# Performance work log

Hardware: AMD Instinct MI355X
Metric: run time of the kernel (lower is better)

The kernel has to match this reference:

```python
import jax, jax.numpy as jnp
import numpy as np

N_HEADS = 16
ROPE_BASE = 10000.0
EPS = float(np.finfo(np.float32).eps)  # F.rms_norm default eps for fp32


def _rms_norm(x):
    # RMSNorm over last dim, no learned scale (modded-nanogpt `norm`)
    return x * jax.lax.rsqrt(jnp.mean(jnp.square(x), axis=-1, keepdims=True) + EPS)


def _rotary(x):
    # x: [B, T, H, D]; non-interleaved half-rotation as in the Rotary module
    B, T, H, D = x.shape
    inv_freq = (1.0 / ROPE_BASE) ** (jnp.arange(0, D, 2, dtype=jnp.float32) / D)  # [D/2]
    t = jnp.arange(T, dtype=jnp.float32)
    freqs = jnp.outer(t, inv_freq)  # [T, D/2]
    cos = jnp.cos(freqs)[None, :, None, :]
    sin = jnp.sin(freqs)[None, :, None, :]
    x1, x2 = jnp.split(x, 2, axis=3)
    y1 = x1 * cos + x2 * sin
    y2 = -x1 * sin + x2 * cos
    return jnp.concatenate((y1, y2), axis=3).astype(x.dtype)


def setup_inputs() -> dict:
    key = jax.random.key(0)
    k1, k2, k3, k4 = jax.random.split(key, 4)
    B, T, Hs = 1, 2048, 2048
    d_head = Hs // N_HEADS
    std = 0.5 * d_head ** (-0.5)
    bound = 3 ** 0.5 * std
    x = jax.random.normal(k1, (B, T, Hs), dtype=jnp.float32)
    Wqkv = jax.random.uniform(k2, (3, Hs, Hs), dtype=jnp.float32, minval=-bound, maxval=bound)
    Wo_w = jax.random.normal(k3, (Hs, Hs), dtype=jnp.float32) * (Hs ** -0.5)
    Wo_b = jax.random.normal(k4, (Hs,), dtype=jnp.float32) * 0.01
    return {"x": x, "Wqkv": Wqkv, "Wo_w": Wo_w, "Wo_b": Wo_b}


def reference(x, Wqkv, Wo_w, Wo_b):
    B, T, Hs = x.shape
    d_head = Hs // N_HEADS
    # fused QKV projection: F.linear(x, Wqkv.flatten(end_dim=1)) -> x @ W^T
    W = Wqkv.reshape(3 * Hs, Hs)
    qkv = jnp.einsum('bth,oh->bto', x, W).reshape(B, T, 3 * N_HEADS, d_head)
    q, k, v = jnp.split(qkv, 3, axis=-2)  # each [B, T, H, D]
    q, k = _rms_norm(q), _rms_norm(k)
    q, k = _rotary(q), _rotary(k)
    # causal attention (flex_attention block_mask = causal), scale = 1/sqrt(d)
    scale = 1.0 / jnp.sqrt(jnp.float32(d_head))
    scores = jnp.einsum('bthd,bshd->bhts', q, k) * scale  # [B, H, T, S]
    causal = jnp.tril(jnp.ones((T, T), dtype=bool))
    scores = jnp.where(causal[None, None], scores, jnp.float32(-1e30))
    probs = jax.nn.softmax(scores, axis=-1)
    y = jnp.einsum('bhts,bshd->bthd', probs, v).reshape(B, T, Hs)
    return jnp.einsum('bth,oh->bto', y, Wo_w) + Wo_b
```

## Files before the change

### kernel.cpp

```cpp
#include <hip/hip_runtime.h>
#include <hip/hip_bf16.h>
#include <stdint.h>

#define T_SEQ 2048
#define HS    2048
#define NH    16
#define DH    128
#define QKVN  (3*HS)

typedef __attribute__((ext_vector_type(8))) short          bf16x8;
typedef __attribute__((ext_vector_type(4))) float          f32x4;
typedef __attribute__((ext_vector_type(4))) unsigned short us4;
typedef __attribute__((ext_vector_type(8))) unsigned short us8;

__device__ __forceinline__ unsigned short f2bf(float x) {
  unsigned int u = __float_as_uint(x);
  return (unsigned short)((u + 0x7fffu + ((u >> 16) & 1u)) >> 16);
}

__device__ __forceinline__ void gl_lds16(const void* g, void* l) {
  __builtin_amdgcn_global_load_lds((__attribute__((address_space(1))) void*)g,
                                   (__attribute__((address_space(3))) void*)l, 16, 0, 0);
}

__global__ __launch_bounds__(256) void cast_bf16_kernel(const float* __restrict__ in,
                                                        unsigned short* __restrict__ out, int n) {
  int i = (blockIdx.x * 256 + threadIdx.x) * 8;
  if (i >= n) return;
  f32x4 a = *(const f32x4*)(in + i);
  f32x4 b = *(const f32x4*)(in + i + 4);
  us8 r;
#pragma unroll
  for (int j = 0; j < 4; ++j) { r[j] = f2bf(a[j]); r[j + 4] = f2bf(b[j]); }
  *(us8*)(out + i) = r;
}

__global__ __launch_bounds__(256) void rope_table_kernel(float* __restrict__ cosd,
                                                         float* __restrict__ sind) {
  int i = blockIdx.x * 256 + threadIdx.x;
  if (i >= T_SEQ * 64) return;
  int t = i >> 6, f = i & 63;
  float inv = expf(-9.210340371976184f * (float)f * (1.0f / 64.0f));
  float ang = (float)t * inv;
  float s, c;
  sincosf(ang, &s, &c);
  cosd[i] = c; sind[i] = s;
}

template <int BIAS, int BN>
__global__ __launch_bounds__(256, 4)
void gemm_bt(const unsigned short* __restrict__ A, const unsigned short* __restrict__ Bt,
             float* __restrict__ C, const float* __restrict__ bias, int M, int N, int K) {
  constexpr int FN = BN / 32;
  __shared__ unsigned short As[128 * 64];
  __shared__ unsigned short Bs[BN * 64];
  const int tid  = threadIdx.x;
  const int lane = tid & 63;
  const int w    = tid >> 6;
  const int fr   = lane & 15;
  const int fq   = lane >> 4;
  const int bm   = blockIdx.y * 128;
  const int bn   = blockIdx.x * BN;
  const int wr   = (w >> 1) * 64;
  const int wc   = (w & 1) * (BN / 2);

  f32x4 acc[4][FN];
#pragma unroll
  for (int m = 0; m < 4; ++m)
#pragma unroll
    for (int n = 0; n < FN; ++n) { acc[m][n][0]=0.f; acc[m][n][1]=0.f; acc[m][n][2]=0.f; acc[m][n][3]=0.f; }

  const int srow = lane >> 3;
  const int sg   = (lane & 7) ^ srow;
  const unsigned short* Ag = A + (long)bm * K;
  const unsigned short* Bg = Bt + (long)bn * K;

  const int nk = K >> 6;
  for (int kt = 0; kt < nk; ++kt) {
    const int k0 = kt << 6;
    __syncthreads();
#pragma unroll
    for (int i = 0; i < 4; ++i) {
      int r = i * 32 + w * 8;
      gl_lds16(Ag + (long)(r + srow) * K + k0 + sg * 8, &As[r * 64]);
    }
#pragma unroll
    for (int i = 0; i < BN / 32; ++i) {
      int r = i * 32 + w * 8;
      gl_lds16(Bg + (long)(r + srow) * K + k0 + sg * 8, &Bs[r * 64]);
    }
    __syncthreads();
    __builtin_amdgcn_s_setprio(1);
#pragma unroll
    for (int ks = 0; ks < 2; ++ks) {
      bf16x8 af[4], bfr[FN];
#pragma unroll
      for (int m = 0; m < 4; ++m)
        af[m]  = *(const bf16x8*)&As[(wr + m * 16 + fr) * 64 + (((ks * 4 + fq) ^ (fr & 7)) << 3)];
#pragma unroll
      for (int n = 0; n < FN; ++n)
        bfr[n] = *(const bf16x8*)&Bs[(wc + n * 16 + fr) * 64 + (((ks * 4 + fq) ^ (fr & 7)) << 3)];
#pragma unroll
      for (int m = 0; m < 4; ++m)
#pragma unroll
        for (int n = 0; n < FN; ++n)
          acc[m][n] = __builtin_amdgcn_mfma_f32_16x16x32_bf16(af[m], bfr[n], acc[m][n], 0, 0, 0);
    }
    __builtin_amdgcn_s_setprio(0);
  }
#pragma unroll
  for (int m = 0; m < 4; ++m) {
    int row0 = bm + wr + m * 16 + fq * 4;
#pragma unroll
    for (int n = 0; n < FN; ++n) {
      int col = bn + wc + n * 16 + fr;
      float bv = BIAS ? bias[col] : 0.0f;
#pragma unroll
      for (int j = 0; j < 4; ++j)
        C[(long)(row0 + j) * N + col] = acc[m][n][j] + bv;
    }
  }
}

__global__ __launch_bounds__(256)
void normrope_qk(const float* __restrict__ qkv, const float* __restrict__ cosd,
                 const float* __restrict__ sind, unsigned short* __restrict__ qb,
                 unsigned short* __restrict__ kb) {
  const int wgl  = (blockIdx.x * 256 + threadIdx.x) >> 6;
  const int lane = threadIdx.x & 63;
  for (int rr = wgl; rr < T_SEQ * 32; rr += 4096) {
    const int t = rr >> 5;
    const int y = rr & 31;
    const float2 v = *(const float2*)(qkv + (long)t * QKVN + y * 128 + lane * 2);
    float ss = v.x * v.x + v.y * v.y;
#pragma unroll
    for (int m = 1; m < 64; m <<= 1) ss += __shfl_xor(ss, m, 64);
    const float r = rsqrtf(ss * (1.0f / 128.0f) + 1.1920928955078125e-07f);
    const float a = v.x * r, b = v.y * r;
    const float pa = __shfl_xor(a, 32, 64), pb = __shfl_xor(b, 32, 64);
    const float2 c2 = *(const float2*)(cosd + t * 64 + (lane & 31) * 2);
    const float2 s2 = *(const float2*)(sind + t * 64 + (lane & 31) * 2);
    float o0, o1;
    if (lane < 32) { o0 =  a * c2.x + pa * s2.x;  o1 =  b * c2.y + pb * s2.y; }
    else           { o0 = -pa * s2.x + a * c2.x;  o1 = -pb * s2.y + b * c2.y; }
    unsigned short* dst = (y >> 4) ? kb : qb;
    const unsigned int packed = (unsigned int)f2bf(o0) | ((unsigned int)f2bf(o1) << 16);
    *(unsigned int*)(dst + ((long)(y & 15) * T_SEQ + t) * 128 + lane * 2) = packed;
  }
}

__global__ __launch_bounds__(256)
void v_transpose(const float* __restrict__ qkv, unsigned short* __restrict__ vt) {
  const int tb = blockIdx.x;
  const int h  = blockIdx.y;
  __shared__ unsigned short vl[128][72];
  const int tid = threadIdx.x;
#pragma unroll
  for (int p = 0; p < 32; ++p) {
    int rr = p * 2 + (tid >> 7);
    int d  = tid & 127;
    float x = qkv[(long)(tb * 64 + rr) * QKVN + 2 * HS + h * 128 + d];
    vl[d][rr] = f2bf(x);
  }
  __syncthreads();
#pragma unroll
  for (int p = 0; p < 8; ++p) {
    int idx = (p * 256 + tid) * 4;
    int d = idx >> 6;
    int i = idx & 63;
    us4 val = *(const us4*)&vl[d][i];
    *(us4*)&vt[((long)h * DH + d) * T_SEQ + tb * 64 + i] = val;
  }
}

__global__ __launch_bounds__(256, 2)
void attn_kernel(const unsigned short* __restrict__ qg, const unsigned short* __restrict__ kg,
                 const unsigned short* __restrict__ vtg, unsigned short* __restrict__ yb) {
  const int bi = blockIdx.x;
  const int j  = (bi < 256) ? bi : bi - 256;
  const int h  = j & 15;
  const int q0 = j >> 4;
  const int qb = (bi < 256) ? (31 - q0) : q0;

  __shared__ unsigned short Ks[2][64 * 128];
  __shared__ unsigned short Vts[2][128 * 64];
  __shared__ unsigned short Ps[4][16 * 72];

  const int tid = threadIdx.x, lane = tid & 63, w = tid >> 6;
  const int fr = lane & 15, fq = lane >> 4;

  const unsigned short* qh = qg  + (long)h * T_SEQ * 128;
  const unsigned short* kh = kg  + (long)h * T_SEQ * 128;
  const unsigned short* vh = vtg + (long)h * 128 * T_SEQ;

  const int krow_off = lane >> 4;
  const int vrow_off = lane >> 3;
  const int vg       = (lane & 7) ^ vrow_off;

  {
#pragma unroll
    for (int i = 0; i < 4; ++i) {
      int c = w * 4 + i;
      int r = 4 * c + krow_off;
      int g = (lane & 15) ^ (r & 7);
      gl_lds16(kh + r * 128 + g * 8, &Ks[0][c * 512]);
    }
#pragma unroll
    for (int i = 0; i < 4; ++i) {
      int r0 = (w * 4 + i) * 8;
      gl_lds16(vh + (long)(r0 + vrow_off) * T_SEQ + vg * 8, &Vts[0][r0 * 64]);
    }
  }

  bf16x8 aq[4];
  {
    const unsigned short* qrow = qh + (long)(qb * 64 + w * 16 + fr) * 128;
#pragma unroll
    for (int ks = 0; ks < 4; ++ks)
      aq[ks] = *(const bf16x8*)(qrow + ks * 32 + fq * 8);
  }

  f32x4 acc[8];
#pragma unroll
  for (int n = 0; n < 8; ++n) { acc[n][0]=0.f; acc[n][1]=0.f; acc[n][2]=0.f; acc[n][3]=0.f; }
  float mrow[4], lrow[4];
#pragma unroll
  for (int j2 = 0; j2 < 4; ++j2) { mrow[j2] = -__builtin_huge_valf(); lrow[j2] = 0.f; }

  const float scale = 0.08838834764831845f;

  __syncthreads();

  for (int kt = 0; kt <= qb; ++kt) {
    const int cur = kt & 1;

    if (kt < qb) {
      const int nb = cur ^ 1;
      const unsigned short* ksrc = kh + (kt + 1) * (64 * 128);
      const unsigned short* vsrc = vh + (kt + 1) * 64;
#pragma unroll
      for (int i = 0; i < 4; ++i) {
        int c = w * 4 + i;
        int r = 4 * c + krow_off;
        int g = (lane & 15) ^ (r & 7);
        gl_lds16(ksrc + r * 128 + g * 8, &Ks[nb][c * 512]);
      }
#pragma unroll
      for (int i = 0; i < 4; ++i) {
        int r0 = (w * 4 + i) * 8;
        gl_lds16(vsrc + (long)(r0 + vrow_off) * T_SEQ + vg * 8, &Vts[nb][r0 * 64]);
      }
    }

    f32x4 sv[4];
#pragma unroll
    for (int n = 0; n < 4; ++n) { sv[n][0]=0.f; sv[n][1]=0.f; sv[n][2]=0.f; sv[n][3]=0.f; }
    __builtin_amdgcn_s_setprio(1);
#pragma unroll
    for (int ks = 0; ks < 4; ++ks)
#pragma unroll
      for (int n = 0; n < 4; ++n) {
        int R = n * 16 + fr;
        bf16x8 bk = *(const bf16x8*)&Ks[cur][R * 128 + (((ks * 4 + fq) ^ (fr & 7)) << 3)];
        sv[n] = __builtin_amdgcn_mfma_f32_16x16x32_bf16(aq[ks], bk, sv[n], 0, 0, 0);
      }
    __builtin_amdgcn_s_setprio(0);

#pragma unroll
    for (int n = 0; n < 4; ++n)
#pragma unroll
      for (int j3 = 0; j3 < 4; ++j3) {
        float s = sv[n][j3] * scale;
        if (kt == qb && (n * 16 + fr) > (w * 16 + fq * 4 + j3)) s = -__builtin_huge_valf();
        sv[n][j3] = s;
      }

    float pm[4];
#pragma unroll
    for (int j3 = 0; j3 < 4; ++j3)
      pm[j3] = fmaxf(fmaxf(sv[0][j3], sv[1][j3]), fmaxf(sv[2][j3], sv[3][j3]));
#pragma unroll
    for (int m = 1; m < 16; m <<= 1)
#pragma unroll
      for (int j3 = 0; j3 < 4; ++j3) pm[j3] = fmaxf(pm[j3], __shfl_xor(pm[j3], m, 64));

    float alpha[4];
#pragma unroll
    for (int j3 = 0; j3 < 4; ++j3) {
      float mn = fmaxf(mrow[j3], pm[j3]);
      alpha[j3] = __expf(mrow[j3] - mn);
      mrow[j3] = mn;
    }
    float rs[4] = {0.f, 0.f, 0.f, 0.f};
#pragma unroll
    for (int n = 0; n < 4; ++n)
#pragma unroll
      for (int j3 = 0; j3 < 4; ++j3) {
        float p = __expf(sv[n][j3] - mrow[j3]);
        sv[n][j3] = p;
        rs[j3] += p;
      }
#pragma unroll
    for (int m = 1; m < 16; m <<= 1)
#pragma unroll
      for (int j3 = 0; j3 < 4; ++j3) rs[j3] += __shfl_xor(rs[j3], m, 64);
#pragma unroll
    for (int j3 = 0; j3 < 4; ++j3) lrow[j3] = lrow[j3] * alpha[j3] + rs[j3];
#pragma unroll
    for (int n = 0; n < 8; ++n)
#pragma unroll
      for (int j3 = 0; j3 < 4; ++j3) acc[n][j3] *= alpha[j3];

    unsigned short* pl = &Ps[w][0];
#pragma unroll
    for (int n = 0; n < 4; ++n)
#pragma unroll
      for (int j3 = 0; j3 < 4; ++j3)
        pl[(fq * 4 + j3) * 72 + n * 16 + fr] = f2bf(sv[n][j3]);
    asm volatile("s_waitcnt lgkmcnt(0)" ::: "memory");
    __builtin_amdgcn_s_setprio(1);
#pragma unroll
    for (int ks = 0; ks < 2; ++ks) {
      bf16x8 pa = *(const bf16x8*)&pl[fr * 72 + ks * 32 + fq * 8];
#pragma unroll
      for (int n = 0; n < 8; ++n) {
        int R = n * 16 + fr;
        bf16x8 bv = *(const bf16x8*)&Vts[cur][R * 64 + (((ks * 4 + fq) ^ (fr & 7)) << 3)];
        acc[n] = __builtin_amdgcn_mfma_f32_16x16x32_bf16(pa, bv, acc[n], 0, 0, 0);
      }
    }
    __builtin_amdgcn_s_setprio(0);

    __syncthreads();
  }

#pragma unroll
  for (int j3 = 0; j3 < 4; ++j3) {
    float inv = 1.0f / lrow[j3];
    int t = qb * 64 + w * 16 + fq * 4 + j3;
#pragma unroll
    for (int n = 0; n < 8; ++n)
      yb[(long)t * HS + h * 128 + n * 16 + fr] = f2bf(acc[n][j3] * inv);
  }
}

extern "C" void kernel_launch(void* const* d_in, const int* in_sizes, int n_in,
                              void* d_out, int out_size, void* d_ws, size_t ws_size,
                              hipStream_t stream) {
  const float* x    = (const float*)d_in[0];
  const float* Wqkv = (const float*)d_in[1];
  const float* Wo_w = (const float*)d_in[2];
  const float* Wo_b = (const float*)d_in[3];
  float* out = (float*)d_out;
  char* ws = (char*)d_ws;

  unsigned short* xbf  = (unsigned short*)(ws + 0L);
  unsigned short* wqbf = (unsigned short*)(ws + 8388608L);
  unsigned short* wobf = (unsigned short*)(ws + 33554432L);
  float*          qkv  = (float*)         (ws + 41943040L);
  unsigned short* qb   = (unsigned short*)(ws + 92274688L);
  unsigned short* kb   = (unsigned short*)(ws + 100663296L);
  unsigned short* vt   = (unsigned short*)(ws + 109051904L);
  unsigned short* yb   = (unsigned short*)(ws + 117440512L);
  float*          cosd = (float*)         (ws + 125829120L);
  float*          sind = (float*)         (ws + 126353408L);

  cast_bf16_kernel<<<dim3(4194304 / 8 / 256), 256, 0, stream>>>(x, xbf, 4194304);
  cast_bf16_kernel<<<dim3(12582912 / 8 / 256), 256, 0, stream>>>(Wqkv, wqbf, 12582912);
  cast_bf16_kernel<<<dim3(4194304 / 8 / 256), 256, 0, stream>>>(Wo_w, wobf, 4194304);
  rope_table_kernel<<<dim3(512), 256, 0, stream>>>(cosd, sind);

  gemm_bt<0, 128><<<dim3(QKVN / 128, T_SEQ / 128), 256, 0, stream>>>(xbf, wqbf, qkv, nullptr,
                                                                     T_SEQ, QKVN, HS);
  normrope_qk<<<dim3(1024), 256, 0, stream>>>(qkv, cosd, sind, qb, kb);
  v_transpose<<<dim3(T_SEQ / 64, NH), 256, 0, stream>>>(qkv, vt);
  attn_kernel<<<dim3(512), 256, 0, stream>>>(qb, kb, vt, yb);
  gemm_bt<1, 64><<<dim3(HS / 64, T_SEQ / 128), 256, 0, stream>>>(yb, wobf, out, Wo_b,
                                                                 T_SEQ, HS, HS);
}
```

Before: 297.4 us.

## Split attention KV loop across two warp groups and merge softmax states

Doubles the attention block to 512 threads, with two groups of four waves each processing alternating 64-key tiles for the same 64-query block using separate double-buffered LDS. At the end the second group writes its partial accumulator and running max/sum to LDS and the first group combines them with a log-sum-exp merge. The aim is to halve the serial KV-loop length per block and raise parallelism. The cost is double the LDS footprint, which may cut occupancy, plus an extra LDS reduction pass. The -inf sentinels are switched to -1e30 so the merge stays finite when a group sees no tiles.

```diff
diff --git a/kernel.cpp b/kernel.cpp
--- a/kernel.cpp
+++ b/kernel.cpp
@@ -173,7 +173,7 @@
   }
 }
 
-__global__ __launch_bounds__(256, 2)
+__global__ __launch_bounds__(512, 2)
 void attn_kernel(const unsigned short* __restrict__ qg, const unsigned short* __restrict__ kg,
                  const unsigned short* __restrict__ vtg, unsigned short* __restrict__ yb) {
   const int bi = blockIdx.x;
@@ -182,11 +182,12 @@
   const int q0 = j >> 4;
   const int qb = (bi < 256) ? (31 - q0) : q0;
 
-  __shared__ unsigned short Ks[2][64 * 128];
-  __shared__ unsigned short Vts[2][128 * 64];
-  __shared__ unsigned short Ps[4][16 * 72];
+  __shared__ unsigned short Ks[2][2][64 * 128];
+  __shared__ unsigned short Vts[2][2][128 * 64];
+  __shared__ unsigned short Ps[8][16 * 72];
 
   const int tid = threadIdx.x, lane = tid & 63, w = tid >> 6;
+  const int g = w >> 2, w4 = w & 3;
   const int fr = lane & 15, fq = lane >> 4;
 
   const unsigned short* qh = qg  + (long)h * T_SEQ * 128;
@@ -197,24 +198,24 @@
   const int vrow_off = lane >> 3;
   const int vg       = (lane & 7) ^ vrow_off;
 
-  {
+  if (g <= qb) {
 #pragma unroll
     for (int i = 0; i < 4; ++i) {
-      int c = w * 4 + i;
+      int c = w4 * 4 + i;
       int r = 4 * c + krow_off;
-      int g = (lane & 15) ^ (r & 7);
-      gl_lds16(kh + r * 128 + g * 8, &Ks[0][c * 512]);
+      int gr = (lane & 15) ^ (r & 7);
+      gl_lds16(kh + (long)g * 8192 + r * 128 + gr * 8, &Ks[g][0][c * 512]);
     }
 #pragma unroll
     for (int i = 0; i < 4; ++i) {
-      int r0 = (w * 4 + i) * 8;
-      gl_lds16(vh + (long)(r0 + vrow_off) * T_SEQ + vg * 8, &Vts[0][r0 * 64]);
+      int r0 = (w4 * 4 + i) * 8;
+      gl_lds16(vh + (long)(r0 + vrow_off) * T_SEQ + g * 64 + vg * 8, &Vts[g][0][r0 * 64]);
     }
   }
 
   bf16x8 aq[4];
   {
-    const unsigned short* qrow = qh + (long)(qb * 64 + w * 16 + fr) * 128;
+    const unsigned short* qrow = qh + (long)(qb * 64 + w4 * 16 + fr) * 128;
 #pragma unroll
     for (int ks = 0; ks < 4; ++ks)
       aq[ks] = *(const bf16x8*)(qrow + ks * 32 + fq * 8);
@@ -225,122 +226,146 @@
   for (int n = 0; n < 8; ++n) { acc[n][0]=0.f; acc[n][1]=0.f; acc[n][2]=0.f; acc[n][3]=0.f; }
   float mrow[4], lrow[4];
 #pragma unroll
-  for (int j2 = 0; j2 < 4; ++j2) { mrow[j2] = -__builtin_huge_valf(); lrow[j2] = 0.f; }
+  for (int j2 = 0; j2 < 4; ++j2) { mrow[j2] = -1e30f; lrow[j2] = 0.f; }
 
   const float scale = 0.08838834764831845f;
+  const int nt = (qb >> 1) + 1;
 
   __syncthreads();
 
-  for (int kt = 0; kt <= qb; ++kt) {
-    const int cur = kt & 1;
-
-    if (kt < qb) {
+  for (int it = 0; it < nt; ++it) {
+    const int cur = it & 1;
+    const int kt  = 2 * it + g;
+
+    if (kt + 2 <= qb) {
       const int nb = cur ^ 1;
-      const unsigned short* ksrc = kh + (kt + 1) * (64 * 128);
-      const unsigned short* vsrc = vh + (kt + 1) * 64;
+      const unsigned short* ksrc = kh + (long)(kt + 2) * 8192;
 #pragma unroll
       for (int i = 0; i < 4; ++i) {
-        int c = w * 4 + i;
+        int c = w4 * 4 + i;
         int r = 4 * c + krow_off;
-        int g = (lane & 15) ^ (r & 7);
-        gl_lds16(ksrc + r * 128 + g * 8, &Ks[nb][c * 512]);
+        int gr = (lane & 15) ^ (r & 7);
+        gl_lds16(ksrc + r * 128 + gr * 8, &Ks[g][nb][c * 512]);
       }
 #pragma unroll
       for (int i = 0; i < 4; ++i) {
-        int r0 = (w * 4 + i) * 8;
-        gl_lds16(vsrc + (long)(r0 + vrow_off) * T_SEQ + vg * 8, &Vts[nb][r0 * 64]);
+        int r0 = (w4 * 4 + i) * 8;
+        gl_lds16(vh + (long)(r0 + vrow_off) * T_SEQ + (kt + 2) * 64 + vg * 8, &Vts[g][nb][r0 * 64]);
       }
     }
 
-    f32x4 sv[4];
-#pragma unroll
-    for (int n = 0; n < 4; ++n) { sv[n][0]=0.f; sv[n][1]=0.f; sv[n][2]=0.f; sv[n][3]=0.f; }
-    __builtin_amdgcn_s_setprio(1);
-#pragma unroll
-    for (int ks = 0; ks < 4; ++ks)
-#pragma unroll
-      for (int n = 0; n < 4; ++n) {
-        int R = n * 16 + fr;
-        bf16x8 bk = *(const bf16x8*)&Ks[cur][R * 128 + (((ks * 4 + fq) ^ (fr & 7)) << 3)];
-        sv[n] = __builtin_amdgcn_mfma_f32_16x16x32_bf16(aq[ks], bk, sv[n], 0, 0, 0);
+    if (kt <= qb) {
+      f32x4 sv[4];
+#pragma unroll
+      for (int n = 0; n < 4; ++n) { sv[n][0]=0.f; sv[n][1]=0.f; sv[n][2]=0.f; sv[n][3]=0.f; }
+      __builtin_amdgcn_s_setprio(1);
+#pragma unroll
+      for (int ks = 0; ks < 4; ++ks)
+#pragma unroll
+        for (int n = 0; n < 4; ++n) {
+          int R = n * 16 + fr;
+          bf16x8 bk = *(const bf16x8*)&Ks[g][cur][R * 128 + (((ks * 4 + fq) ^ (fr & 7)) << 3)];
+          sv[n] = __builtin_amdgcn_mfma_f32_16x16x32_bf16(aq[ks], bk, sv[n], 0, 0, 0);
+        }
+      __builtin_amdgcn_s_setprio(0);
+
+#pragma unroll
+      for (int n = 0; n < 4; ++n)
+#pragma unroll
+        for (int j3 = 0; j3 < 4; ++j3) {
+          float s = sv[n][j3] * scale;
+          if (kt == qb && (n * 16 + fr) > (w4 * 16 + fq * 4 + j3)) s = -1e30f;
+          sv[n][j3] = s;
+        }
+
+      float pm[4];
+#pragma unroll
+      for (int j3 = 0; j3 < 4; ++j3)
+        pm[j3] = fmaxf(fmaxf(sv[0][j3], sv[1][j3]), fmaxf(sv[2][j3], sv[3][j3]));
+#pragma unroll
+      for (int m = 1; m < 16; m <<= 1)
+#pragma unroll
+        for (int j3 = 0; j3 < 4; ++j3) pm[j3] = fmaxf(pm[j3], __shfl_xor(pm[j3], m, 64));
+
+      float alpha[4];
+#pragma unroll
+      for (int j3 = 0; j3 < 4; ++j3) {
+        float mn = fmaxf(mrow[j3], pm[j3]);
+        alpha[j3] = __expf(mrow[j3] - mn);
+        mrow[j3] = mn;
       }
-    __builtin_amdgcn_s_setprio(0);
-
-#pragma unroll
-    for (int n = 0; n < 4; ++n)
-#pragma unroll
-      for (int j3 = 0; j3 < 4; ++j3) {
-        float s = sv[n][j3] * scale;
-        if (kt == qb && (n * 16 + fr) > (w * 16 + fq * 4 + j3)) s = -__builtin_huge_valf();
-        sv[n][j3] = s;
+      float rs[4] = {0.f, 0.f, 0.f, 0.f};
+#pragma unroll
+      for (int n = 0; n < 4; ++n)
+#pragma unroll
+        for (int j3 = 0; j3 < 4; ++j3) {
+          float p = __expf(sv[n][j3] - mrow[j3]);
+          sv[n][j3] = p;
+          rs[j3] += p;
+        }
+#pragma unroll
+      for (int m = 1; m < 16; m <<= 1)
+#pragma unroll
+        for (int j3 = 0; j3 < 4; ++j3) rs[j3] += __shfl_xor(rs[j3], m, 64);
+#pragma unroll
+      for (int j3 = 0; j3 < 4; ++j3) lrow[j3] = lrow[j3] * alpha[j3] + rs[j3];
+#pragma unroll
+      for (int n = 0; n < 8; ++n)
+#pragma unroll
+        for (int j3 = 0; j3 < 4; ++j3) acc[n][j3] *= alpha[j3];
+
+      unsigned short* pl = &Ps[w][0];
+#pragma unroll
+      for (int n = 0; n < 4; ++n)
+#pragma unroll
+        for (int j3 = 0; j3 < 4; ++j3)
+          pl[(fq * 4 + j3) * 72 + n * 16 + fr] = f2bf(sv[n][j3]);
+      asm volatile("s_waitcnt lgkmcnt(0)" ::: "memory");
+      __builtin_amdgcn_s_setprio(1);
+#pragma unroll
+      for (int ks = 0; ks < 2; ++ks) {
+        bf16x8 pa = *(const bf16x8*)&pl[fr * 72 + ks * 32 + fq * 8];
+#pragma unroll
+        for (int n = 0; n < 8; ++n) {
+          int R = n * 16 + fr;
+          bf16x8 bv = *(const bf16x8*)&Vts[g][cur][R * 64 + (((ks * 4 + fq) ^ (fr & 7)) << 3)];
+          acc[n] = __builtin_amdgcn_mfma_f32_16x16x32_bf16(pa, bv, acc[n], 0, 0, 0);
+        }
       }
-
-    float pm[4];
-#pragma unroll
-    for (int j3 = 0; j3 < 4; ++j3)
-      pm[j3] = fmaxf(fmaxf(sv[0][j3], sv[1][j3]), fmaxf(sv[2][j3], sv[3][j3]));
-#pragma unroll
-    for (int m = 1; m < 16; m <<= 1)
-#pragma unroll
-      for (int j3 = 0; j3 < 4; ++j3) pm[j3] = fmaxf(pm[j3], __shfl_xor(pm[j3], m, 64));
-
-    float alpha[4];
+      __builtin_amdgcn_s_setprio(0);
+    }
+
+    __syncthreads();
+  }
+
+  float* accL = (float*)&Ks[1][0][0];
+  float* mlL  = (float*)&Vts[1][0][0];
+  if (g == 1) {
 #pragma unroll
     for (int j3 = 0; j3 < 4; ++j3) {
-      float mn = fmaxf(mrow[j3], pm[j3]);
-      alpha[j3] = __expf(mrow[j3] - mn);
-      mrow[j3] = mn;
-    }
-    float rs[4] = {0.f, 0.f, 0.f, 0.f};
-#pragma unroll
-    for (int n = 0; n < 4; ++n)
-#pragma unroll
-      for (int j3 = 0; j3 < 4; ++j3) {
-        float p = __expf(sv[n][j3] - mrow[j3]);
-        sv[n][j3] = p;
-        rs[j3] += p;
+      int row = w4 * 16 + fq * 4 + j3;
+#pragma unroll
+      for (int n = 0; n < 8; ++n)
+        accL[row * 128 + n * 16 + fr] = acc[n][j3];
+      if (fr == 0) { mlL[row] = mrow[j3]; mlL[64 + row] = lrow[j3]; }
+    }
+  }
+  __syncthreads();
+  if (g == 0) {
+#pragma unroll
+    for (int j3 = 0; j3 < 4; ++j3) {
+      int row = w4 * 16 + fq * 4 + j3;
+      float m1 = mlL[row], l1 = mlL[64 + row];
+      float m  = fmaxf(mrow[j3], m1);
+      float a0 = __expf(mrow[j3] - m), a1 = __expf(m1 - m);
+      float inv = 1.0f / (lrow[j3] * a0 + l1 * a1);
+      int t = qb * 64 + row;
+#pragma unroll
+      for (int n = 0; n < 8; ++n) {
+        float v = (acc[n][j3] * a0 + accL[row * 128 + n * 16 + fr] * a1) * inv;
+        yb[(long)t * HS + h * 128 + n * 16 + fr] = f2bf(v);
       }
-#pragma unroll
-    for (int m = 1; m < 16; m <<= 1)
-#pragma unroll
-      for (int j3 = 0; j3 < 4; ++j3) rs[j3] += __shfl_xor(rs[j3], m, 64);
-#pragma unroll
-    for (int j3 = 0; j3 < 4; ++j3) lrow[j3] = lrow[j3] * alpha[j3] + rs[j3];
-#pragma unroll
-    for (int n = 0; n < 8; ++n)
-#pragma unroll
-      for (int j3 = 0; j3 < 4; ++j3) acc[n][j3] *= alpha[j3];
-
-    unsigned short* pl = &Ps[w][0];
-#pragma unroll
-    for (int n = 0; n < 4; ++n)
-#pragma unroll
-      for (int j3 = 0; j3 < 4; ++j3)
-        pl[(fq * 4 + j3) * 72 + n * 16 + fr] = f2bf(sv[n][j3]);
-    asm volatile("s_waitcnt lgkmcnt(0)" ::: "memory");
-    __builtin_amdgcn_s_setprio(1);
-#pragma unroll
-    for (int ks = 0; ks < 2; ++ks) {
-      bf16x8 pa = *(const bf16x8*)&pl[fr * 72 + ks * 32 + fq * 8];
-#pragma unroll
-      for (int n = 0; n < 8; ++n) {
-        int R = n * 16 + fr;
-        bf16x8 bv = *(const bf16x8*)&Vts[cur][R * 64 + (((ks * 4 + fq) ^ (fr & 7)) << 3)];
-        acc[n] = __builtin_amdgcn_mfma_f32_16x16x32_bf16(pa, bv, acc[n], 0, 0, 0);
-      }
-    }
-    __builtin_amdgcn_s_setprio(0);
-
-    __syncthreads();
-  }
-
-#pragma unroll
-  for (int j3 = 0; j3 < 4; ++j3) {
-    float inv = 1.0f / lrow[j3];
-    int t = qb * 64 + w * 16 + fq * 4 + j3;
-#pragma unroll
-    for (int n = 0; n < 8; ++n)
-      yb[(long)t * HS + h * 128 + n * 16 + fr] = f2bf(acc[n][j3] * inv);
+    }
   }
 }
 
@@ -374,7 +399,7 @@
                                                                      T_SEQ, QKVN, HS);
   normrope_qk<<<dim3(1024), 256, 0, stream>>>(qkv, cosd, sind, qb, kb);
   v_transpose<<<dim3(T_SEQ / 64, NH), 256, 0, stream>>>(qkv, vt);
-  attn_kernel<<<dim3(512), 256, 0, stream>>>(qb, kb, vt, yb);
+  attn_kernel<<<dim3(512), 512, 0, stream>>>(qb, kb, vt, yb);
   gemm_bt<1, 64><<<dim3(HS / 64, T_SEQ / 128), 256, 0, stream>>>(yb, wobf, out, Wo_b,
                                                                  T_SEQ, HS, HS);
 }
```

After: 290.2 us. 1.02x faster.

## Split causal attention KV range in two and merge partials in combine kernel

Applied to the files above, without the earlier changes.

Each (query block, head) attention task is split into two halves of its causal KV range, doubling the grid to 1024 blocks. Each block writes unnormalized fp32 accumulators plus running max and sum to workspace. A new combine kernel rescales and merges the two partials into bf16 output. This shortens the longest per-block serial loop and improves load balance across CUs, at the cost of an extra launch and roughly 32 MB of fp32 partial traffic written and read back through reused workspace regions.

```diff
diff --git a/kernel.cpp b/kernel.cpp
--- a/kernel.cpp
+++ b/kernel.cpp
@@ -175,20 +175,38 @@
 
 __global__ __launch_bounds__(256, 2)
 void attn_kernel(const unsigned short* __restrict__ qg, const unsigned short* __restrict__ kg,
-                 const unsigned short* __restrict__ vtg, unsigned short* __restrict__ yb) {
+                 const unsigned short* __restrict__ vtg, float* __restrict__ accG,
+                 float* __restrict__ mlG) {
   const int bi = blockIdx.x;
-  const int j  = (bi < 256) ? bi : bi - 256;
-  const int h  = j & 15;
-  const int q0 = j >> 4;
-  const int qb = (bi < 256) ? (31 - q0) : q0;
+  const int q0 = (bi & 255) >> 4;
+  const int h  = bi & 15;
+  const int quarter = bi >> 8;
+  const int qb = (quarter < 2) ? (31 - q0) : q0;
+  const int p  = quarter & 1;
+  const int slot = (qb * 16 + h) * 2 + p;
+
+  const int kt0 = p ? ((qb >> 1) + 1) : 0;
+  const int kte = p ? qb : (qb >> 1);
+
+  const int tid = threadIdx.x, lane = tid & 63, w = tid >> 6;
+  const int fr = lane & 15, fq = lane >> 4;
+
+  float* accO = accG + (long)slot * 8192;
+  float* mlO  = mlG + slot * 128;
+
+  if (kt0 > kte) {
+#pragma unroll
+    for (int j3 = 0; j3 < 4; ++j3) {
+      int row = w * 16 + fq * 4 + j3;
+      if (fr == 0) { mlO[row] = -1e30f; mlO[64 + row] = 0.f; }
+    }
+    return;
+  }
 
   __shared__ unsigned short Ks[2][64 * 128];
   __shared__ unsigned short Vts[2][128 * 64];
   __shared__ unsigned short Ps[4][16 * 72];
 
-  const int tid = threadIdx.x, lane = tid & 63, w = tid >> 6;
-  const int fr = lane & 15, fq = lane >> 4;
-
   const unsigned short* qh = qg  + (long)h * T_SEQ * 128;
   const unsigned short* kh = kg  + (long)h * T_SEQ * 128;
   const unsigned short* vh = vtg + (long)h * 128 * T_SEQ;
@@ -198,17 +216,18 @@
   const int vg       = (lane & 7) ^ vrow_off;
 
   {
+    const unsigned short* ksrc = kh + (long)kt0 * 8192;
 #pragma unroll
     for (int i = 0; i < 4; ++i) {
       int c = w * 4 + i;
       int r = 4 * c + krow_off;
-      int g = (lane & 15) ^ (r & 7);
-      gl_lds16(kh + r * 128 + g * 8, &Ks[0][c * 512]);
+      int gr = (lane & 15) ^ (r & 7);
+      gl_lds16(ksrc + r * 128 + gr * 8, &Ks[0][c * 512]);
     }
 #pragma unroll
     for (int i = 0; i < 4; ++i) {
       int r0 = (w * 4 + i) * 8;
-      gl_lds16(vh + (long)(r0 + vrow_off) * T_SEQ + vg * 8, &Vts[0][r0 * 64]);
+      gl_lds16(vh + (long)(r0 + vrow_off) * T_SEQ + kt0 * 64 + vg * 8, &Vts[0][r0 * 64]);
     }
   }
 
@@ -225,30 +244,29 @@
   for (int n = 0; n < 8; ++n) { acc[n][0]=0.f; acc[n][1]=0.f; acc[n][2]=0.f; acc[n][3]=0.f; }
   float mrow[4], lrow[4];
 #pragma unroll
-  for (int j2 = 0; j2 < 4; ++j2) { mrow[j2] = -__builtin_huge_valf(); lrow[j2] = 0.f; }
+  for (int j2 = 0; j2 < 4; ++j2) { mrow[j2] = -1e30f; lrow[j2] = 0.f; }
 
   const float scale = 0.08838834764831845f;
 
   __syncthreads();
 
-  for (int kt = 0; kt <= qb; ++kt) {
-    const int cur = kt & 1;
-
-    if (kt < qb) {
+  for (int kt = kt0; kt <= kte; ++kt) {
+    const int cur = (kt - kt0) & 1;
+
+    if (kt < kte) {
       const int nb = cur ^ 1;
-      const unsigned short* ksrc = kh + (kt + 1) * (64 * 128);
-      const unsigned short* vsrc = vh + (kt + 1) * 64;
+      const unsigned short* ksrc = kh + (long)(kt + 1) * 8192;
 #pragma unroll
       for (int i = 0; i < 4; ++i) {
         int c = w * 4 + i;
         int r = 4 * c + krow_off;
-        int g = (lane & 15) ^ (r & 7);
-        gl_lds16(ksrc + r * 128 + g * 8, &Ks[nb][c * 512]);
+        int gr = (lane & 15) ^ (r & 7);
+        gl_lds16(ksrc + r * 128 + gr * 8, &Ks[nb][c * 512]);
       }
 #pragma unroll
       for (int i = 0; i < 4; ++i) {
         int r0 = (w * 4 + i) * 8;
-        gl_lds16(vsrc + (long)(r0 + vrow_off) * T_SEQ + vg * 8, &Vts[nb][r0 * 64]);
+        gl_lds16(vh + (long)(r0 + vrow_off) * T_SEQ + (kt + 1) * 64 + vg * 8, &Vts[nb][r0 * 64]);
       }
     }
 
@@ -271,7 +289,7 @@
 #pragma unroll
       for (int j3 = 0; j3 < 4; ++j3) {
         float s = sv[n][j3] * scale;
-        if (kt == qb && (n * 16 + fr) > (w * 16 + fq * 4 + j3)) s = -__builtin_huge_valf();
+        if (kt == qb && (n * 16 + fr) > (w * 16 + fq * 4 + j3)) s = -1e30f;
         sv[n][j3] = s;
       }
 
@@ -296,9 +314,9 @@
     for (int n = 0; n < 4; ++n)
 #pragma unroll
       for (int j3 = 0; j3 < 4; ++j3) {
-        float p = __expf(sv[n][j3] - mrow[j3]);
-        sv[n][j3] = p;
-        rs[j3] += p;
+        float pval = __expf(sv[n][j3] - mrow[j3]);
+        sv[n][j3] = pval;
+        rs[j3] += pval;
       }
 #pragma unroll
     for (int m = 1; m < 16; m <<= 1)
@@ -336,11 +354,41 @@
 
 #pragma unroll
   for (int j3 = 0; j3 < 4; ++j3) {
-    float inv = 1.0f / lrow[j3];
-    int t = qb * 64 + w * 16 + fq * 4 + j3;
+    int row = w * 16 + fq * 4 + j3;
 #pragma unroll
     for (int n = 0; n < 8; ++n)
-      yb[(long)t * HS + h * 128 + n * 16 + fr] = f2bf(acc[n][j3] * inv);
+      accO[row * 128 + n * 16 + fr] = acc[n][j3];
+    if (fr == 0) { mlO[row] = mrow[j3]; mlO[64 + row] = lrow[j3]; }
+  }
+}
+
+__global__ __launch_bounds__(256)
+void attn_combine(const float* __restrict__ accG, const float* __restrict__ mlG,
+                  unsigned short* __restrict__ yb) {
+  const int j = blockIdx.x;
+  const int qb = j >> 4, h = j & 15;
+  const float* a0 = accG + (long)(j * 2 + 0) * 8192;
+  const float* a1 = accG + (long)(j * 2 + 1) * 8192;
+  const float* ml0 = mlG + (j * 2 + 0) * 128;
+  const float* ml1 = mlG + (j * 2 + 1) * 128;
+  const int tid = threadIdx.x;
+#pragma unroll
+  for (int e = 0; e < 8; ++e) {
+    int idx = e * 256 + tid;
+    int row = idx >> 5;
+    int c4  = (idx & 31) * 4;
+    float m0 = ml0[row], l0 = ml0[64 + row];
+    float m1 = ml1[row], l1 = ml1[64 + row];
+    float m  = fmaxf(m0, m1);
+    float w0 = __expf(m0 - m), w1 = __expf(m1 - m);
+    float inv = 1.0f / (l0 * w0 + l1 * w1);
+    f32x4 A = *(const f32x4*)(a0 + row * 128 + c4);
+    f32x4 B = *(const f32x4*)(a1 + row * 128 + c4);
+    us4 o;
+#pragma unroll
+    for (int q = 0; q < 4; ++q)
+      o[q] = f2bf((A[q] * w0 + B[q] * w1) * inv);
+    *(us4*)(yb + (long)(qb * 64 + row) * HS + h * 128 + c4) = o;
   }
 }
 
@@ -364,6 +412,8 @@
   unsigned short* yb   = (unsigned short*)(ws + 117440512L);
   float*          cosd = (float*)         (ws + 125829120L);
   float*          sind = (float*)         (ws + 126353408L);
+  float*          accG = (float*)         (ws + 0L);
+  float*          mlG  = (float*)         (ws + 41943040L);
 
   cast_bf16_kernel<<<dim3(4194304 / 8 / 256), 256, 0, stream>>>(x, xbf, 4194304);
   cast_bf16_kernel<<<dim3(12582912 / 8 / 256), 256, 0, stream>>>(Wqkv, wqbf, 12582912);
@@ -374,7 +424,8 @@
                                                                      T_SEQ, QKVN, HS);
   normrope_qk<<<dim3(1024), 256, 0, stream>>>(qkv, cosd, sind, qb, kb);
   v_transpose<<<dim3(T_SEQ / 64, NH), 256, 0, stream>>>(qkv, vt);
-  attn_kernel<<<dim3(512), 256, 0, stream>>>(qb, kb, vt, yb);
+  attn_kernel<<<dim3(1024), 256, 0, stream>>>(qb, kb, vt, accG, mlG);
+  attn_combine<<<dim3(512), 256, 0, stream>>>(accG, mlG, yb);
   gemm_bt<1, 64><<<dim3(HS / 64, T_SEQ / 128), 256, 0, stream>>>(yb, wobf, out, Wo_b,
                                                                  T_SEQ, HS, HS);
 }
```

Result: faster. 289.1 us (-2.8%).
